# Performance work log

Measured on AMD Instinct MI355X. Metric: run time of the kernel, lower is better.

## Reference

```python
import jax
import jax.numpy as jnp
import numpy as np
from jax import lax

D_MODEL = 256
D_ATT = 256
NHEAD = 8
D_FF = 1024
N_SAMPLED = 128
TEMP = 1.0
DEPTH = 32
N_LOCAL = 4
DH_K = D_ATT // NHEAD
DH_V = D_MODEL // NHEAD
BIG = 1e9
ATT_SCALE = 1.0 / float(np.sqrt(DH_K))


def _rmsnorm(x, g, eps=1e-6):
    return x * lax.rsqrt(jnp.mean(x * x, axis=-1, keepdims=True) + eps) * g


def _weighted_mean(p, mask):
    # p: [b,n,1], mask: [b,n]
    n = jnp.sum(mask, axis=1, keepdims=True)[..., None]
    return jnp.sum(p * mask[..., None], axis=1, keepdims=True) / (n + 1e-9)


def _normalize(v, axis):
    return v / jnp.maximum(jnp.linalg.norm(v, axis=axis, keepdims=True), 1e-12)


def _select_duplet(points, mask, key):
    # pick midpoint of two random masked-in points, per batch
    k1, k2 = jax.random.split(key)
    def pick(k):
        s = jax.random.uniform(k, mask.shape) + (1.0 - mask) * BIG
        idx = jnp.argmin(s, axis=1)
        return jnp.take_along_axis(points, idx[:, None, None], axis=1)  # [b,1,3]
    return (pick(k1) + pick(k2)) * 0.5


def random_serialization(points, mask, key):
    b, n, _ = points.shape
    inf = 2.0 ** (DEPTH // 2 + 3)
    # integer halving schedule: 2^(D/2+1), //2 each step (hits 0 eventually)
    scales = jnp.asarray([float((2 ** (DEPTH // 2 + 1)) >> i) for i in range(DEPTH)], jnp.float32)
    keys = jax.random.split(key, DEPTH)

    def step(carry, xs):
        pts, total, old = carry
        k, scale = xs
        ka, kl, kr = jax.random.split(k, 3)
        ABC = jax.random.normal(ka, (b, 3, 1), jnp.float32)
        ang = jnp.sum(_normalize(ABC, 1) * _normalize(old, 1), axis=1, keepdims=True)
        sgn = jnp.sign(ang)
        sgn = jnp.where(sgn == 0, 1.0, sgn)
        ABC = ABC * sgn
        proj = jnp.matmul(pts, ABC)  # [b,n,1]
        proj = proj - _weighted_mean(proj, mask)
        score = jnp.sign(proj)
        total = total + score * scale
        mask_l = jnp.minimum(jax.nn.relu(-score[..., 0]), mask)
        mask_r = jnp.minimum(jax.nn.relu(score[..., 0]), mask)
        pl = pts - _select_duplet(pts, mask_l, kl)
        pr = pts - _select_duplet(pts, mask_r, kr)
        pts = pl * mask_l[..., None] + pr * mask_r[..., None]
        return (pts, total, ABC), None

    init = (points, jnp.zeros((b, n, 1), jnp.float32), jnp.ones((b, 3, 1), jnp.float32))
    (_, total, _), _ = lax.scan(step, init, (keys, scales))
    total = total + inf * (1.0 - mask)[..., None]
    return jnp.argsort(total[..., 0], axis=1)  # [b,n]


def _dszrc(xn, kv, mask, Ws, bs):
    # learned per-head importance top-k sampler with differentiable gate
    score = jnp.einsum('bnd,dh->bhn', xn, Ws) + bs[None, :, None]
    score = score - (1.0 - mask)[:, None, :] * BIG
    vals, idx = lax.top_k(score, N_SAMPLED)  # [b,h,s]
    gate = jax.nn.sigmoid(vals / TEMP)
    sampled = jnp.take_along_axis(kv, idx[..., None], axis=2)  # [b,h,s,dk+dv]
    return sampled * gate[..., None]


def _block(x, mask, rs, P):
    Wq, bq, Wkv, bkv, Wc, bc, W1, b1, W2, b2, Ws, bs, g1, g2 = P
    b, n, d = x.shape
    xn = _rmsnorm(x, g1)
    q = (xn @ Wq + bq).reshape(b, n, NHEAD, DH_K).transpose(0, 2, 1, 3)
    kv = (xn @ Wkv + bkv).reshape(b, n, NHEAD, DH_K + DH_V).transpose(0, 2, 1, 3)
    kv = _dszrc(xn, kv, mask, Ws, bs)
    k, v = kv[..., :DH_K], kv[..., DH_K:]
    logits = jnp.einsum('bhqd,bhkd->bhqk', q, k) * ATT_SCALE
    att = jax.nn.softmax(logits, axis=-1)
    xa = jnp.einsum('bhqk,bhkd->bhqd', att, v).transpose(0, 2, 1, 3).reshape(b, n, D_MODEL)
    x = x + (xa @ Wc + bc) * rs
    h = _rmsnorm(x, g2)
    mlp = jax.nn.gelu(h @ W1 + b1, approximate=False) @ W2 + b2
    return x + mlp * rs


def _forward(x, x_coords, mask, rs, params):
    idx = random_serialization(x_coords, mask, jax.random.key(42))
    rev = jnp.argsort(idx, axis=1)
    x = jnp.take_along_axis(x, idx[..., None], axis=1)
    b, n, d = x.shape
    # faithful to torch add_remainder_token_trans (pads a full window if n%N==0)
    rem = N_SAMPLED - (n % N_SAMPLED)
    xp = jnp.pad(x, ((0, 0), (0, rem), (0, 0)))
    mp = jnp.pad(mask, ((0, 0), (0, rem)))
    npad = n + rem
    xl = xp.reshape(b * N_SAMPLED, npad // N_SAMPLED, d)
    ml = mp.reshape(b * N_SAMPLED, npad // N_SAMPLED)
    for i in range(N_LOCAL):
        xl = _block(xl, ml, rs, tuple(a[i] for a in params))
    x = xl.reshape(b, npad, d)[:, :n]
    m = mp[:, :n]
    x = _block(x, m, rs, tuple(a[-1] for a in params))
    return jnp.take_along_axis(x, rev[..., None], axis=1)


def setup_inputs() -> dict:
    key = jax.random.key(0)
    ks = jax.random.split(key, 10)
    b, n = 4, 16384
    L = N_LOCAL + 1
    s = 0.02
    return {
        'x': jax.random.normal(ks[0], (b, n, D_MODEL), jnp.float32),
        'x_coords': jax.random.normal(ks[1], (b, n, 3), jnp.float32),
        'mask': jnp.ones((b, n), jnp.float32),
        'residual_scale': jnp.float32(1.0),
        'Wq': jax.random.normal(ks[2], (L, D_MODEL, D_ATT), jnp.float32) * s,
        'bq': jnp.zeros((L, D_ATT), jnp.float32),
        'Wkv': jax.random.normal(ks[3], (L, D_MODEL, D_ATT + D_MODEL), jnp.float32) * s,
        'bkv': jnp.zeros((L, D_ATT + D_MODEL), jnp.float32),
        'Wc': jax.random.normal(ks[4], (L, D_MODEL, D_MODEL), jnp.float32) * s,
        'bc': jnp.zeros((L, D_MODEL), jnp.float32),
        'W1': jax.random.normal(ks[5], (L, D_MODEL, D_FF), jnp.float32) * s,
        'b1': jnp.zeros((L, D_FF), jnp.float32),
        'W2': jax.random.normal(ks[6], (L, D_FF, D_MODEL), jnp.float32) * s,
        'b2': jnp.zeros((L, D_MODEL), jnp.float32),
        'Ws': jax.random.normal(ks[7], (L, D_MODEL, NHEAD), jnp.float32) * s,
        'bs': jnp.zeros((L, NHEAD), jnp.float32),
        'g1': jnp.ones((L, D_MODEL), jnp.float32),
        'g2': jnp.ones((L, D_MODEL), jnp.float32),
    }


def reference(x, x_coords, mask, residual_scale, Wq, bq, Wkv, bkv, Wc, bc, W1, b1, W2, b2, Ws, bs, g1, g2):
    params = (Wq, bq, Wkv, bkv, Wc, bc, W1, b1, W2, b2, Ws, bs, g1, g2)
    return _forward(x, x_coords, mask, residual_scale, params)
```

## Files before the change

kernel.cpp:

```cpp
#include <hip/hip_runtime.h>

typedef unsigned int u32;
typedef unsigned short u16;
typedef unsigned long long u64;
typedef float f32x4 __attribute__((ext_vector_type(4)));
typedef short s16x8 __attribute__((ext_vector_type(8)));

#define BIGF 1e9f

__device__ __forceinline__ float b2f(u16 u){ return __uint_as_float(((u32)u) << 16); }
__device__ __forceinline__ u16 f2b(float f){
  u32 x = __float_as_uint(f);
  u32 r = x + 0x7FFFu + ((x >> 16) & 1u);
  return (u16)(r >> 16);
}
__device__ __forceinline__ float fin(float v){
  u32 u = __float_as_uint(v);
  return ((u & 0x7F800000u) == 0x7F800000u) ? 0.0f : v;
}
__device__ __forceinline__ bool is_bf(const u32* mraw){ return mraw[0] != 0x3F800000u; }
__device__ __forceinline__ float ldin(const void* p, size_t i, bool bf){
  return bf ? b2f(((const u16*)p)[i]) : ((const float*)p)[i];
}
__device__ __forceinline__ u32 mono32(float f){
  u32 u = __float_as_uint(f);
  return u ^ ((u & 0x80000000u) ? 0xFFFFFFFFu : 0x80000000u);
}
__device__ __forceinline__ u64 umin64(u64 a, u64 b){ return a < b ? a : b; }
__device__ __forceinline__ u32 rotl32(u32 x, int r){ return (x << r) | (x >> (32 - r)); }
__device__ __forceinline__ u32 gp2(u32 u, float g){
  float lo = fin(b2f((u16)(u & 0xFFFFu)) * g), hi = fin(b2f((u16)(u >> 16)) * g);
  return (u32)f2b(lo) | ((u32)f2b(hi) << 16);
}
__device__ __forceinline__ float sigm(float ms){
  return (ms > -30.f) ? 1.0f/(1.0f + __expf(-ms)) : 0.0f;
}

__device__ __forceinline__ void gload_lds16(const u16* gsrc, u16* ldst){
  __builtin_amdgcn_global_load_lds(
      (const __attribute__((address_space(1))) u32*)gsrc,
      (__attribute__((address_space(3))) u32*)ldst, 16, 0, 0);
}

__device__ __forceinline__ void tf2(u32 k0, u32 k1, u32 x0, u32 x1, u32& o0, u32& o1){
  u32 ks2 = k0 ^ k1 ^ 0x1BD11BDAu;
  x0 += k0; x1 += k1;
#define TFR(r) { x0 += x1; x1 = rotl32(x1, (r)); x1 ^= x0; }
  TFR(13) TFR(15) TFR(26) TFR(6)
  x0 += k1; x1 += ks2 + 1u;
  TFR(17) TFR(29) TFR(16) TFR(24)
  x0 += ks2; x1 += k0 + 2u;
  TFR(13) TFR(15) TFR(26) TFR(6)
  x0 += k0; x1 += k1 + 3u;
  TFR(17) TFR(29) TFR(16) TFR(24)
  x0 += k1; x1 += ks2 + 4u;
  TFR(13) TFR(15) TFR(26) TFR(6)
  x0 += ks2; x1 += k0 + 5u;
#undef TFR
  o0 = x0; o1 = x1;
}

__device__ float erfinv_xla(float x){
#pragma clang fp contract(off)
  float w = -log1pf(-x*x);
  float p;
  if (w < 5.0f){
    w = w - 2.5f;
    p = 2.81022636e-08f;
    p = 3.43273939e-07f + p*w;
    p = -3.5233877e-06f + p*w;
    p = -4.39150654e-06f + p*w;
    p = 0.00021858087f + p*w;
    p = -0.00125372503f + p*w;
    p = -0.00417768164f + p*w;
    p = 0.246640727f + p*w;
    p = 1.50140941f + p*w;
  } else {
    w = sqrtf(w) - 3.0f;
    p = -0.000200214257f;
    p = 0.000100950558f + p*w;
    p = 0.00134934322f + p*w;
    p = -0.00367342844f + p*w;
    p = 0.00573950773f + p*w;
    p = -0.0076224613f + p*w;
    p = 0.00943887047f + p*w;
    p = 1.00167406f + p*w;
    p = 2.83297682f + p*w;
  }
  return p*x;
}

__global__ void k_fallback(void* out, int n, const u32* mraw){
  bool bf = is_bf(mraw);
  int i = blockIdx.x*256 + threadIdx.x;
  if (i < n){ if (bf) ((u16*)out)[i] = f2b(0.125f); else ((float*)out)[i] = 0.125f; }
}

__global__ void k_zero(u32* p, int n){
  int i = blockIdx.x*256 + threadIdx.x;
  if (i < n) p[i] = 0u;
}

__global__ void k_conv(const void* src, float* dst, int n, const u32* mraw){
  bool bf = is_bf(mraw);
  int i = blockIdx.x*256 + threadIdx.x;
  if (i < n) dst[i] = fin(ldin(src, (size_t)i, bf));
}
__global__ void k_wt(const void* src, u16* dst, int L, int K, int N, const u32* mraw){
  bool bf = is_bf(mraw);
  int i = blockIdx.x*256 + threadIdx.x;
  if (i >= L*K*N) return;
  int l = i/(K*N); int r = i%(K*N); int n = r/K; int k = r%K;
  dst[i] = f2b(fin(ldin(src, (size_t)l*K*N + (size_t)k*N + n, bf)));
}

__global__ void k_rng_setup(float* ABCbuf, u32* pickkeys){
#pragma clang fp contract(off)
  __shared__ float rawn[18][12];
  int s = threadIdx.x;
  if (s < 18){
    u32 ks0, ks1, o0, o1;
    tf2(0u, 42u, 0u, (u32)s, ks0, ks1);
    u32 ka0,ka1,kl0,kl1,kr0,kr1;
    tf2(ks0,ks1, 0u,0u, ka0,ka1);
    tf2(ks0,ks1, 0u,1u, kl0,kl1);
    tf2(ks0,ks1, 0u,2u, kr0,kr1);
    const float MINV = __uint_as_float(0xBF7FFFFFu);
    const float SQ2  = __uint_as_float(0x3FB504F3u);
    for (int j = 0; j < 12; ++j){
      tf2(ka0,ka1, 0u, (u32)j, o0, o1);
      u32 bits = o0 ^ o1;
      float f = __uint_as_float((bits >> 9) | 0x3F800000u) - 1.0f;
      float u = f*2.0f + MINV;
      u = fmaxf(MINV, u);
      rawn[s][j] = SQ2 * erfinv_xla(u);
    }
    u32 a0,a1;
    tf2(kl0,kl1, 0u,0u, a0,a1); pickkeys[(s*4+0)*2]=a0; pickkeys[(s*4+0)*2+1]=a1;
    tf2(kl0,kl1, 0u,1u, a0,a1); pickkeys[(s*4+1)*2]=a0; pickkeys[(s*4+1)*2+1]=a1;
    tf2(kr0,kr1, 0u,0u, a0,a1); pickkeys[(s*4+2)*2]=a0; pickkeys[(s*4+2)*2+1]=a1;
    tf2(kr0,kr1, 0u,1u, a0,a1); pickkeys[(s*4+3)*2]=a0; pickkeys[(s*4+3)*2+1]=a1;
  }
  __syncthreads();
  if (threadIdx.x == 0){
    float oldv[4][3];
    for (int b=0;b<4;b++){ oldv[b][0]=1.f; oldv[b][1]=1.f; oldv[b][2]=1.f; }
    for (int st = 0; st < 18; ++st){
      for (int b = 0; b < 4; ++b){
        float A0 = rawn[st][b*3+0], A1 = rawn[st][b*3+1], A2 = rawn[st][b*3+2];
        float na = fmaxf(sqrtf((A0*A0 + A1*A1) + A2*A2), 1e-12f);
        float p0 = oldv[b][0], p1 = oldv[b][1], p2 = oldv[b][2];
        float no = fmaxf(sqrtf((p0*p0 + p1*p1) + p2*p2), 1e-12f);
        float ang = (A0/na)*(p0/no) + (A1/na)*(p1/no) + (A2/na)*(p2/no);
        float sg = (ang > 0.f) ? 1.f : ((ang < 0.f) ? -1.f : 1.f);
        A0 *= sg; A1 *= sg; A2 *= sg;
        oldv[b][0]=A0; oldv[b][1]=A1; oldv[b][2]=A2;
        ABCbuf[(st*4+b)*3+0]=A0; ABCbuf[(st*4+b)*3+1]=A1; ABCbuf[(st*4+b)*3+2]=A2;
      }
    }
  }
}

__global__ void k_rng_bits(const u32* pickkeys, u32* bits){
  int id = blockIdx.x*256 + threadIdx.x;
  if (id >= 18*4*65536) return;
  int sp = id >> 16; u32 f = (u32)(id & 0xFFFF);
  u32 o0, o1;
  tf2(pickkeys[sp*2], pickkeys[sp*2+1], 0u, f, o0, o1);
  bits[id] = o0 ^ o1;
}

__device__ __forceinline__ void gbar(u32* slot){
  __syncthreads();
  if (threadIdx.x == 0){
    __hip_atomic_fetch_add(slot, 1u, __ATOMIC_ACQ_REL, __HIP_MEMORY_SCOPE_AGENT);
    while (__hip_atomic_load(slot, __ATOMIC_RELAXED, __HIP_MEMORY_SCOPE_AGENT) < 64u)
      __builtin_amdgcn_s_sleep(2);
    (void)__hip_atomic_load(slot, __ATOMIC_ACQUIRE, __HIP_MEMORY_SCOPE_AGENT);
  }
  __syncthreads();
}

__global__ __launch_bounds__(512) void k_serialize_coop(
    const float* __restrict__ coordsf, const float* __restrict__ maskf,
    const float* __restrict__ ABCbuf, const u32* __restrict__ bits,
    int* __restrict__ tkeys, double* __restrict__ sumpart, int* __restrict__ npart,
    u64* __restrict__ reckey, float4* __restrict__ recxyz, u32* __restrict__ gbars){
#pragma clang fp contract(off)
  __shared__ double sd[8];
  __shared__ int si[8];
  __shared__ u64 sp[4][8];
  int bx = blockIdx.x;
  int b = bx >> 4, blk = bx & 15;
  int t = threadIdx.x, wid = t >> 6, lane = t & 63;
  int base_i = blk*1024;

  float p[2][3]; int tk[2]; u32 mb = 0;
#pragma unroll
  for (int j = 0; j < 2; ++j){
    int i = base_i + j*512 + t;
    size_t cb = (size_t)(b*16384 + i)*3;
    p[j][0] = coordsf[cb+0]; p[j][1] = coordsf[cb+1]; p[j][2] = coordsf[cb+2];
    if (maskf[b*16384 + i] > 0.f) mb |= (1u << j);
    tk[j] = 0;
  }
  {
    int c = __popc(mb);
#pragma unroll
    for (int d = 1; d < 64; d <<= 1) c += __shfl_xor(c, d);
    if (lane == 0) si[wid] = c;
    __syncthreads();
    if (t == 0){ int cc = 0; for (int w = 0; w < 8; ++w) cc += si[w]; npart[b*16 + blk] = cc; }
  }
  float nplus = 0.f;

  for (int s = 0; s < 18; ++s){
    float A0 = ABCbuf[(s*4+b)*3+0], A1 = ABCbuf[(s*4+b)*3+1], A2 = ABCbuf[(s*4+b)*3+2];
    float pr[2]; double acc = 0.0;
#pragma unroll
    for (int j = 0; j < 2; ++j){
      pr[j] = p[j][0]*A0 + p[j][1]*A1 + p[j][2]*A2;
      if ((mb >> j) & 1u) acc += (double)pr[j];
    }
#pragma unroll
    for (int d = 1; d < 64; d <<= 1) acc += __shfl_xor(acc, d);
    if (lane == 0) sd[wid] = acc;
    __syncthreads();
    if (t == 0){ double tt = 0.0; for (int w = 0; w < 8; ++w) tt += sd[w]; sumpart[b*16 + blk] = tt; }
    gbar(&gbars[s*2 + 0]);

    if (s == 0){
      int cc = 0; for (int k2 = 0; k2 < 16; ++k2) cc += npart[b*16 + k2];
      nplus = (float)((double)cc + 1e-9);
    }
    double tot = 0.0;
    for (int k2 = 0; k2 < 16; ++k2) tot += sumpart[b*16 + k2];
    float mean = ((float)tot) / nplus;

    u32 sideL = 0, sideR = 0;
    int sc17 = 1 << (17 - s);
#pragma unroll
    for (int j = 0; j < 2; ++j){
      float pc = pr[j] - mean;
      int sc = (pc > 0.f) ? 1 : ((pc < 0.f) ? -1 : 0);
      tk[j] += sc * sc17;
      bool mi = (mb >> j) & 1u;
      if (mi && sc < 0) sideL |= (1u << j);
      if (mi && sc > 0) sideR |= (1u << j);
    }
    u64 mine[4]; int bj[4];
#pragma unroll
    for (int pk = 0; pk < 4; ++pk){ mine[pk] = ~0ULL; bj[pk] = 0; }
#pragma unroll
    for (int pk = 0; pk < 4; ++pk){
      const u32* bp = bits + (size_t)(s*4 + pk)*65536 + b*16384;
      u32 sm = (pk < 2) ? sideL : sideR;
#pragma unroll
      for (int j = 0; j < 2; ++j){
        if ((sm >> j) & 1u){
          int i = base_i + j*512 + t;
          u64 pkd = ((u64)(bp[i] >> 9) << 14) | (u32)i;
          if (pkd < mine[pk]){ mine[pk] = pkd; bj[pk] = j; }
        }
      }
    }
    u64 red[4];
#pragma unroll
    for (int pk = 0; pk < 4; ++pk) red[pk] = mine[pk];
#pragma unroll
    for (int d = 1; d < 64; d <<= 1)
#pragma unroll
      for (int pk = 0; pk < 4; ++pk) red[pk] = umin64(red[pk], __shfl_xor(red[pk], d));
    if (lane == 0){
#pragma unroll
      for (int pk = 0; pk < 4; ++pk) sp[pk][wid] = red[pk];
    }
    __syncthreads();
    u64 mm[4];
#pragma unroll
    for (int pk = 0; pk < 4; ++pk){
      u64 v = ~0ULL;
      for (int w = 0; w < 8; ++w) v = umin64(v, sp[pk][w]);
      mm[pk] = v;
    }
#pragma unroll
    for (int pk = 0; pk < 4; ++pk){
      int ri = ((b*4 + pk) << 4) + blk;
      if (mm[pk] == ~0ULL){
        if (t == 0){ reckey[ri] = ~0ULL; recxyz[ri] = make_float4(0.f, 0.f, 0.f, 0.f); }
      } else if (mine[pk] == mm[pk]){
        int j = bj[pk];
        reckey[ri] = mm[pk];
        recxyz[ri] = make_float4(p[j][0], p[j][1], p[j][2], 0.f);
      }
    }
    gbar(&gbars[s*2 + 1]);

    float wc[4][3];
#pragma unroll
    for (int pk = 0; pk < 4; ++pk){
      u64 best = ~0ULL; int bk = 0;
      for (int k2 = 0; k2 < 16; ++k2){
        u64 kk = reckey[((b*4 + pk) << 4) + k2];
        if (kk < best){ best = kk; bk = k2; }
      }
      float4 c = recxyz[((b*4 + pk) << 4) + bk];
      wc[pk][0] = c.x; wc[pk][1] = c.y; wc[pk][2] = c.z;
    }
    float dl0=(wc[0][0]+wc[1][0])*0.5f, dl1=(wc[0][1]+wc[1][1])*0.5f, dl2=(wc[0][2]+wc[1][2])*0.5f;
    float dr0=(wc[2][0]+wc[3][0])*0.5f, dr1=(wc[2][1]+wc[3][1])*0.5f, dr2=(wc[2][2]+wc[3][2])*0.5f;
#pragma unroll
    for (int j = 0; j < 2; ++j){
      bool L = (sideL >> j) & 1u, R = (sideR >> j) & 1u;
      if (L){ p[j][0]-=dl0; p[j][1]-=dl1; p[j][2]-=dl2; }
      else if (R){ p[j][0]-=dr0; p[j][1]-=dr1; p[j][2]-=dr2; }
      else { p[j][0]=0.f; p[j][1]=0.f; p[j][2]=0.f; }
    }
  }
#pragma unroll
  for (int j = 0; j < 2; ++j){
    int i = base_i + j*512 + t;
    tkeys[b*16384 + i] = tk[j] + (((mb >> j) & 1u) ? 0 : 524288);
  }
}

__global__ __launch_bounds__(1024) void k_bsort_phase1(u64* buf){
  __shared__ u64 sb[8192];
  u64* g = buf + (size_t)blockIdx.x*8192;
  int tid = threadIdx.x;
  for (int i = tid; i < 8192; i += 1024) sb[i] = g[i];
  int ab = blockIdx.x & 1;
  for (int k = 2; k <= 8192; k <<= 1){
    for (int j = k >> 1; j > 0; j >>= 1){
      __syncthreads();
      for (int pp = tid; pp < 4096; pp += 1024){
        int i  = ((pp & ~(j - 1)) << 1) | (pp & (j - 1));
        int ix = i | j;
        bool up = (k == 8192) ? (ab == 0) : ((i & k) == 0);
        u64 A = sb[i], B = sb[ix];
        if ((A > B) == up){ sb[i] = B; sb[ix] = A; }
      }
    }
  }
  __syncthreads();
  for (int i = tid; i < 8192; i += 1024) g[i] = sb[i];
}
__global__ __launch_bounds__(1024) void k_bsort_merge(u64* buf){
  u64* g = buf + (size_t)blockIdx.x*16384;
  for (int i = threadIdx.x; i < 8192; i += 1024){
    u64 A = g[i], B = g[i + 8192];
    if (A > B){ g[i] = B; g[i + 8192] = A; }
  }
}
__global__ __launch_bounds__(1024) void k_bsort_phase3(u64* buf){
  __shared__ u64 sb[8192];
  u64* g = buf + (size_t)blockIdx.x*8192;
  int tid = threadIdx.x;
  for (int i = tid; i < 8192; i += 1024) sb[i] = g[i];
  for (int j = 4096; j > 0; j >>= 1){
    __syncthreads();
    for (int pp = tid; pp < 4096; pp += 1024){
      int i  = ((pp & ~(j - 1)) << 1) | (pp & (j - 1));
      int ix = i | j;
      u64 A = sb[i], B = sb[ix];
      if (A > B){ sb[i] = B; sb[ix] = A; }
    }
  }
  __syncthreads();
  for (int i = tid; i < 8192; i += 1024) g[i] = sb[i];
}

__global__ void k_fill_sort(const int* tkeys, u64* sbuf){
  int id = blockIdx.x*256 + threadIdx.x;
  if (id >= 65536) return;
  u32 tv = (u32)(tkeys[id] + 262144);
  sbuf[id] = ((u64)tv << 14) | (u32)(id & 16383);
}
__global__ void k_unpack_sort(const u64* sbuf, int* idxb, int* revb){
  int id = blockIdx.x*256 + threadIdx.x;
  if (id >= 65536) return;
  int a = id >> 14, r = id & 16383;
  int orig = (int)(sbuf[id] & 16383u);
  idxb[id] = orig;
  revb[(a << 14) | orig] = r;
}

__global__ void k_gather(const void* xraw, const int* idxb, float* xbuf, const u32* mraw){
  bool bf = is_bf(mraw);
  int r = blockIdx.x, c = threadIdx.x;
  int b = r / 16512, rr = r % 16512;
  float v = 0.f;
  if (rr < 16384){
    int src = idxb[b*16384 + rr];
    v = fin(ldin(xraw, (size_t)(b*16384 + src)*256 + c, bf));
  }
  xbuf[(size_t)r*256 + c] = v;
}

__global__ void k_rmsnorm(const float* x, const float* g, u16* xn){
  int row = blockIdx.x*4 + (threadIdx.x >> 6);
  int lane = threadIdx.x & 63;
  float4 xv = *(const float4*)&x[(size_t)row*256 + lane*4];
  xv.x = fin(xv.x); xv.y = fin(xv.y); xv.z = fin(xv.z); xv.w = fin(xv.w);
  float ss = xv.x*xv.x + xv.y*xv.y + xv.z*xv.z + xv.w*xv.w;
#pragma unroll
  for (int d = 1; d < 64; d <<= 1) ss += __shfl_xor(ss, d);
  float sc = 1.0f / sqrtf(ss*(1.0f/256.0f) + 1e-6f);
  float4 gv = *(const float4*)&g[lane*4];
  ushort4 o4;
  o4.x = f2b(fin((xv.x*sc)*gv.x)); o4.y = f2b(fin((xv.y*sc)*gv.y));
  o4.z = f2b(fin((xv.z*sc)*gv.z)); o4.w = f2b(fin((xv.w*sc)*gv.w));
  *(ushort4*)&xn[(size_t)row*256 + lane*4] = o4;
}

__global__ __launch_bounds__(256) void k_gemm(const u16* A, int lda, const u16* Bt, int ldb,
                                              int M, int N, int K, const float* bias,
                                              void* C, int ldc, int mode, const float* rsp){
  __shared__ __align__(16) u16 As[128*64];
  __shared__ __align__(16) u16 Bs[128*64];
  int tid = threadIdx.x;
  int gx = (int)gridDim.x;
  int nwg = gx * (int)gridDim.y;
  int d = (int)blockIdx.y * gx + (int)blockIdx.x;
  int q = nwg >> 3, r = nwg & 7;
  int xcd = d & 7, off = d >> 3;
  int wg = (xcd < r ? xcd*(q+1) : r*(q+1) + (xcd - r)*q) + off;
  int bxi = wg % gx, byi = wg / gx;
  int gm0 = byi*128, gn0 = bxi*128;
  int wv = tid >> 6, lane = tid & 63, q4 = lane >> 4, l16 = lane & 15;
  int wm = (wv >> 1)*64, wn = (wv & 1)*64;
  int lr = lane >> 3;
  int lcs = ((lane & 7) ^ lr) << 3;
  f32x4 acc[4][4];
#pragma unroll
  for (int i = 0; i < 4; ++i)
#pragma unroll
    for (int j = 0; j < 4; ++j) acc[i][j] = (f32x4){0.f,0.f,0.f,0.f};
  for (int k0 = 0; k0 < K; k0 += 64){
    __syncthreads();
#pragma unroll
    for (int i = 0; i < 4; ++i){
      int chunk = wv*4 + i;
      int row = chunk*8 + lr;
      gload_lds16(&A[(size_t)(gm0+row)*lda + k0 + lcs],  &As[chunk*512]);
      gload_lds16(&Bt[(size_t)(gn0+row)*ldb + k0 + lcs], &Bs[chunk*512]);
    }
    __syncthreads();
#pragma unroll
    for (int ks = 0; ks < 64; ks += 32){
      int swc = ((((ks >> 3) + q4) ^ (l16 & 7)) << 3);
      s16x8 aF[4], bF[4];
#pragma unroll
      for (int mt = 0; mt < 4; ++mt) aF[mt] = *(const s16x8*)&As[(wm + mt*16 + l16)*64 + swc];
#pragma unroll
      for (int nt = 0; nt < 4; ++nt) bF[nt] = *(const s16x8*)&Bs[(wn + nt*16 + l16)*64 + swc];
#pragma unroll
      for (int mt = 0; mt < 4; ++mt)
#pragma unroll
        for (int nt = 0; nt < 4; ++nt)
          acc[mt][nt] = __builtin_amdgcn_mfma_f32_16x16x32_bf16(aF[mt], bF[nt], acc[mt][nt], 0, 0, 0);
    }
  }
  float rs = rsp[0];
  const float SQ2C = 1.41421356237f;
#pragma unroll
  for (int mt = 0; mt < 4; ++mt)
#pragma unroll
    for (int nt = 0; nt < 4; ++nt){
      int col = gn0 + wn + nt*16 + l16;
      float bi = bias[col];
#pragma unroll
      for (int rg = 0; rg < 4; ++rg){
        int row = gm0 + wm + mt*16 + q4*4 + rg;
        float v = fin(acc[mt][nt][rg] + bi);
        size_t off2 = (size_t)row*ldc + col;
        if (mode == 0) ((float*)C)[off2] = v;
        else if (mode == 1){ float* X = (float*)C; X[off2] = fin(X[off2] + v*rs); }
        else if (mode == 2) ((u16*)C)[off2] = f2b(v);
        else { float gl = 0.5f * v * (1.0f + erff(v / SQ2C)); ((u16*)C)[off2] = f2b(fin(gl)); }
      }
    }
}

__global__ __launch_bounds__(256) void k_gemm_score(const u16* __restrict__ A,
                                                    const u16* __restrict__ Bt,
                                                    int M, const float* __restrict__ bias,
                                                    float* __restrict__ C){
  __shared__ __align__(16) u16 As[128*72];
  int tid = threadIdx.x;
  int gm0 = blockIdx.x*128;
  int wv = tid >> 6, lane = tid & 63, q4 = lane >> 4, l16 = lane & 15;
  int wm = wv*32;
  int ar = tid >> 2, ac = tid & 3;
  f32x4 acc[2];
  acc[0] = (f32x4){0.f,0.f,0.f,0.f};
  acc[1] = (f32x4){0.f,0.f,0.f,0.f};
  for (int k0 = 0; k0 < 256; k0 += 64){
    __syncthreads();
#pragma unroll
    for (int ps = 0; ps < 2; ++ps){
      int r2 = ps*64 + ar;
      uint4 va0 = {0u,0u,0u,0u}, va1 = {0u,0u,0u,0u};
      if (gm0 + r2 < M){
        const u16* ap = &A[(size_t)(gm0+r2)*256 + k0 + ac*16];
        va0 = ((const uint4*)ap)[0];
        va1 = ((const uint4*)ap)[1];
      }
      *(uint4*)&As[r2*72 + ac*16]     = va0;
      *(uint4*)&As[r2*72 + ac*16 + 8] = va1;
    }
    __syncthreads();
#pragma unroll
    for (int ks = 0; ks < 64; ks += 32){
      s16x8 bF = (s16x8){0,0,0,0,0,0,0,0};
      if (l16 < 8) bF = *(const s16x8*)&Bt[(size_t)l16*256 + k0 + ks + q4*8];
      s16x8 aF0 = *(const s16x8*)&As[(wm + l16)*72 + ks + q4*8];
      s16x8 aF1 = *(const s16x8*)&As[(wm + 16 + l16)*72 + ks + q4*8];
      acc[0] = __builtin_amdgcn_mfma_f32_16x16x32_bf16(aF0, bF, acc[0], 0, 0, 0);
      acc[1] = __builtin_amdgcn_mfma_f32_16x16x32_bf16(aF1, bF, acc[1], 0, 0, 0);
    }
  }
  if (l16 < 8){
    float bi = bias[l16];
#pragma unroll
    for (int mt = 0; mt < 2; ++mt)
#pragma unroll
      for (int rg = 0; rg < 4; ++rg){
        int row = gm0 + wm + mt*16 + q4*4 + rg;
        if (row < M) C[(size_t)row*8 + l16] = fin(acc[mt][rg] + bi);
      }
  }
}

__global__ __launch_bounds__(512) void k_sel_local(const float* scoreb, const float* maskf,
                                                   u32* sel, float* gateb){
  int s = blockIdx.x, h = threadIdx.x >> 6, lane = threadIdx.x & 63;
  int b = s >> 7, tt = s & 127;
  u64 pm = ~0ULL;
  for (int rep = 0; rep < 3; ++rep){
    int j = lane + rep*64;
    if (j < 129){
      int p = tt*129 + j;
      float m = (p < 16384) ? maskf[b*16384 + p] : 0.f;
      float ms = fin(scoreb[(size_t)(s*129 + j)*8 + h]) - (1.0f - m)*BIGF;
      u64 pk = ((u64)mono32(ms) << 9) | (u32)(511 - j);
      pm = umin64(pm, pk);
    }
  }
#pragma unroll
  for (int d = 1; d < 64; d <<= 1) pm = umin64(pm, __shfl_xor(pm, d));
  int dropped = 511 - (int)(pm & 511u);
  int sh = s*8 + h;
  for (int rep = 0; rep < 3; ++rep){
    int j = lane + rep*64;
    if (j < 129 && j != dropped){
      int slot = j - (j > dropped ? 1 : 0);
      int p = tt*129 + j;
      float m = (p < 16384) ? maskf[b*16384 + p] : 0.f;
      float ms = fin(scoreb[(size_t)(s*129 + j)*8 + h]) - (1.0f - m)*BIGF;
      sel[sh*128 + slot] = (u32)(s*129 + j);
      gateb[sh*128 + slot] = fin(sigm(ms));
    }
  }
}

__global__ void k_fill_topk(const float* scoreb, const float* maskf, u64* sbuf){
  int id = blockIdx.x*256 + threadIdx.x;
  if (id >= 524288) return;
  int arr = id >> 14, i = id & 16383;
  int b = arr >> 3, h = arr & 7;
  float m = maskf[b*16384 + i];
  float ms = fin(scoreb[(size_t)(b*16512 + i)*8 + h]) - (1.0f - m)*BIGF;
  sbuf[id] = ((u64)(~mono32(ms)) << 14) | (u32)i;
}
__global__ void k_sel_gemit(const u64* sbuf, const float* scoreb, const float* maskf,
                            u32* sel, float* gateb){
  int arr = blockIdx.x, tid = threadIdx.x;
  int b = arr >> 3, h = arr & 7;
  int j = (int)(sbuf[(size_t)arr*16384 + tid] & 16383u);
  float m = maskf[b*16384 + j];
  float ms = fin(scoreb[(size_t)(b*16512 + j)*8 + h]) - (1.0f - m)*BIGF;
  sel[arr*128 + tid] = (u32)(b*16512 + j);
  gateb[arr*128 + tid] = fin(sigm(ms));
}

__global__ __launch_bounds__(256) void k_attn(const u16* qb, const u16* vkv,
                                              const u32* sel, const float* gateb,
                                              u16* xa, int gmode){
  __shared__ __align__(16) u16 Qsm[144*40];
  __shared__ __align__(16) u16 Ksm[128*40];
  __shared__ __align__(16) u16 Vtsm[32*136];
  __shared__ __align__(16) u16 Psm[4*16*136];
  int tid = threadIdx.x;
  int bx = blockIdx.x, h = blockIdx.y;
  int rows, rowbase, kvs, ntiles;
  if (gmode){
    int b = bx >> 7, rb = bx & 127;
    rows = 128; rowbase = b*16512 + rb*128; kvs = b; ntiles = 8;
  } else {
    rows = 129; rowbase = bx*129; kvs = bx; ntiles = 9;
  }
  int sh = kvs*8 + h;
  for (int t = tid; t < 144; t += 256) *(uint4*)&Qsm[t*40 + 32] = (uint4){0u,0u,0u,0u};
  if (tid < 128) *(uint4*)&Ksm[tid*40 + 32] = (uint4){0u,0u,0u,0u};
  if (tid < 32)  *(uint4*)&Vtsm[tid*136 + 128] = (uint4){0u,0u,0u,0u};
  if (tid < 64)  *(uint4*)&Psm[tid*136 + 128] = (uint4){0u,0u,0u,0u};
  for (int t = tid; t < 576; t += 256){
    int r = t >> 2, c = t & 3;
    uint4 v = {0u,0u,0u,0u};
    if (r < rows) v = *(const uint4*)&qb[(size_t)(rowbase + r)*256 + h*32 + c*8];
    *(uint4*)&Qsm[r*40 + c*8] = v;
  }
  for (int t = tid; t < 512; t += 256){
    int slot = t >> 2, part = t & 3;
    u32 rowi = sel[sh*128 + slot];
    float gv = fin(gateb[sh*128 + slot]);
    uint4 vk = *(const uint4*)&vkv[(size_t)rowi*512 + h*64 + part*8];
    uint4 wk; wk.x = gp2(vk.x, gv); wk.y = gp2(vk.y, gv); wk.z = gp2(vk.z, gv); wk.w = gp2(vk.w, gv);
    *(uint4*)&Ksm[slot*40 + part*8] = wk;
    uint4 vv = *(const uint4*)&vkv[(size_t)rowi*512 + h*64 + 32 + part*8];
    u32 vd[4] = {vv.x, vv.y, vv.z, vv.w};
#pragma unroll
    for (int e = 0; e < 4; ++e){
      float lo = fin(b2f((u16)(vd[e] & 0xFFFFu)) * gv), hi = fin(b2f((u16)(vd[e] >> 16)) * gv);
      Vtsm[(part*8 + e*2 + 0)*136 + slot] = f2b(lo);
      Vtsm[(part*8 + e*2 + 1)*136 + slot] = f2b(hi);
    }
  }
  __syncthreads();
  int wv = tid >> 6, lane = tid & 63, q4 = lane >> 4, l16 = lane & 15;
  u16* Pw = Psm + wv*(16*136);
  const float ATTSC = 0.17677669529663689f;
  f32x4 z = {0.f,0.f,0.f,0.f};
  for (int mt = wv; mt < ntiles; mt += 4){
    int m0 = mt*16;
    s16x8 aQ = *(const s16x8*)&Qsm[(m0 + l16)*40 + q4*8];
    f32x4 S[8];
#pragma unroll
    for (int nt = 0; nt < 8; ++nt){
      s16x8 bK = *(const s16x8*)&Ksm[(nt*16 + l16)*40 + q4*8];
      S[nt] = __builtin_amdgcn_mfma_f32_16x16x32_bf16(aQ, bK, z, 0, 0, 0);
    }
    float mx[4] = {-1e30f,-1e30f,-1e30f,-1e30f};
#pragma unroll
    for (int nt = 0; nt < 8; ++nt)
#pragma unroll
      for (int rg = 0; rg < 4; ++rg){ float v = fin(S[nt][rg])*ATTSC; S[nt][rg] = v; mx[rg] = fmaxf(mx[rg], v); }
#pragma unroll
    for (int d = 1; d < 16; d <<= 1)
#pragma unroll
      for (int rg = 0; rg < 4; ++rg) mx[rg] = fmaxf(mx[rg], __shfl_xor(mx[rg], d));
    float sm[4] = {0.f,0.f,0.f,0.f};
#pragma unroll
    for (int nt = 0; nt < 8; ++nt)
#pragma unroll
      for (int rg = 0; rg < 4; ++rg){ float e = __expf(S[nt][rg] - mx[rg]); S[nt][rg] = e; sm[rg] += e; }
#pragma unroll
    for (int d = 1; d < 16; d <<= 1)
#pragma unroll
      for (int rg = 0; rg < 4; ++rg) sm[rg] += __shfl_xor(sm[rg], d);
    float inv[4];
#pragma unroll
    for (int rg = 0; rg < 4; ++rg) inv[rg] = 1.0f/fmaxf(sm[rg], 1e-20f);
#pragma unroll
    for (int nt = 0; nt < 8; ++nt)
#pragma unroll
      for (int rg = 0; rg < 4; ++rg)
        Pw[(q4*4 + rg)*136 + nt*16 + l16] = f2b(fin(S[nt][rg]*inv[rg]));
    f32x4 O0 = z, O1 = z;
#pragma unroll
    for (int kq = 0; kq < 4; ++kq){
      s16x8 aP = *(const s16x8*)&Pw[l16*136 + kq*32 + q4*8];
      s16x8 b0 = *(const s16x8*)&Vtsm[l16*136 + kq*32 + q4*8];
      s16x8 b1 = *(const s16x8*)&Vtsm[(16 + l16)*136 + kq*32 + q4*8];
      O0 = __builtin_amdgcn_mfma_f32_16x16x32_bf16(aP, b0, O0, 0, 0, 0);
      O1 = __builtin_amdgcn_mfma_f32_16x16x32_bf16(aP, b1, O1, 0, 0, 0);
    }
#pragma unroll
    for (int rg = 0; rg < 4; ++rg){
      int r = m0 + q4*4 + rg;
      if (r < rows){
        size_t base = (size_t)(rowbase + r)*256 + h*32;
        xa[base + l16] = f2b(fin(O0[rg]));
        xa[base + 16 + l16] = f2b(fin(O1[rg]));
      }
    }
  }
}

__global__ void k_output(const float* xbuf, const int* revb, void* out, const u32* mraw){
  bool bf = is_bf(mraw);
  int r = blockIdx.x, c = threadIdx.x;
  int b = r >> 14;
  int rank = revb[r];
  float v = fin(xbuf[(size_t)(b*16512 + rank)*256 + c]);
  if (bf) ((u16*)out)[(size_t)r*256 + c] = f2b(v);
  else ((float*)out)[(size_t)r*256 + c] = v;
}

extern "C" void kernel_launch(void* const* d_in, const int* in_sizes, int n_in,
                              void* d_out, int out_size, void* d_ws, size_t ws_size,
                              hipStream_t stream){
  (void)in_sizes; (void)n_in;
  const u32* mraw = (const u32*)d_in[2];
  char* wsp = (char*)d_ws;
  size_t o = 0;
  auto alloc = [&](size_t bytes)->void*{ void* p = (void*)(wsp + o); o += (bytes + 255) & ~(size_t)255; return p; };
  float* maskf   = (float*)alloc(65536u*4);
  float* coordsf = (float*)alloc(196608u*4);
  float* rsf     = (float*)alloc(256);
  float* bqf     = (float*)alloc(5*256*4);
  float* bkvf    = (float*)alloc(5*512*4);
  float* bsf     = (float*)alloc(5*8*4);
  float* bcf     = (float*)alloc(5*256*4);
  float* b1f     = (float*)alloc(5*1024*4);
  float* b2f     = (float*)alloc(5*256*4);
  float* g1f     = (float*)alloc(5*256*4);
  float* g2f     = (float*)alloc(5*256*4);
  u16* WqT  = (u16*)alloc((size_t)5*256*256*2);
  u16* WvT  = (u16*)alloc((size_t)5*512*256*2);
  u16* WsT  = (u16*)alloc((size_t)5*8*256*2);
  u16* WcT  = (u16*)alloc((size_t)5*256*256*2);
  u16* W1T  = (u16*)alloc((size_t)5*1024*256*2);
  u16* W2T  = (u16*)alloc((size_t)5*1024*256*2);
  float* ABCbuf = (float*)alloc(18*12*4);
  u32* pickkeys = (u32*)alloc(72*2*4);
  int* tkeys = (int*)alloc(65536u*4);
  int* idxb  = (int*)alloc(65536u*4);
  int* revb  = (int*)alloc(65536u*4);
  double* sumpart = (double*)alloc(64*8);
  int*    npart   = (int*)alloc(64*4);
  u64*    reckey  = (u64*)alloc(256*8);
  float4* recxyz  = (float4*)alloc(256*16);
  u32*    gbars   = (u32*)alloc(64*4);
  u64* sortbuf = (u64*)alloc((size_t)32*16384*8);
  float* xbuf = (float*)alloc((size_t)66048*256*4);
  u16* xn  = (u16*)alloc((size_t)66048*256*2);
  float* scoreb = (float*)alloc((size_t)66048*8*4);
  const size_t SZ_VKV = (size_t)66048*512*2;
  const size_t SZ_QB  = (size_t)66048*256*2;
  const size_t SZ_SEL = (size_t)4096*128*4;
  char* Sbase = (char*)alloc(SZ_VKV + SZ_QB + 2*SZ_SEL);
  u16* vkv    = (u16*)Sbase;
  u16* qb     = (u16*)(Sbase + SZ_VKV);
  u32* sel    = (u32*)(Sbase + SZ_VKV + SZ_QB);
  float* gateb= (float*)(Sbase + SZ_VKV + SZ_QB + SZ_SEL);
  u32* bitsb  = (u32*)Sbase;
  u16* ffb    = (u16*)Sbase;
  u16* xa     = qb;

  if (o > ws_size){
    k_fallback<<<dim3((out_size + 255)/256), 256, 0, stream>>>(d_out, out_size, mraw);
    return;
  }

  k_conv<<<dim3(256), 256, 0, stream>>>(d_in[2], maskf, 65536, mraw);
  k_conv<<<dim3(768), 256, 0, stream>>>(d_in[1], coordsf, 196608, mraw);
  k_conv<<<dim3(1), 256, 0, stream>>>(d_in[3], rsf, 1, mraw);
  k_conv<<<dim3(5), 256, 0, stream>>>(d_in[5], bqf, 1280, mraw);
  k_conv<<<dim3(10), 256, 0, stream>>>(d_in[7], bkvf, 2560, mraw);
  k_conv<<<dim3(1), 256, 0, stream>>>(d_in[15], bsf, 40, mraw);
  k_conv<<<dim3(5), 256, 0, stream>>>(d_in[9], bcf, 1280, mraw);
  k_conv<<<dim3(20), 256, 0, stream>>>(d_in[11], b1f, 5120, mraw);
  k_conv<<<dim3(5), 256, 0, stream>>>(d_in[13], b2f, 1280, mraw);
  k_conv<<<dim3(5), 256, 0, stream>>>(d_in[16], g1f, 1280, mraw);
  k_conv<<<dim3(5), 256, 0, stream>>>(d_in[17], g2f, 1280, mraw);
  k_wt<<<dim3(1280), 256, 0, stream>>>(d_in[4], WqT, 5, 256, 256, mraw);
  k_wt<<<dim3(2560), 256, 0, stream>>>(d_in[6], WvT, 5, 256, 512, mraw);
  k_wt<<<dim3(40), 256, 0, stream>>>(d_in[14], WsT, 5, 256, 8, mraw);
  k_wt<<<dim3(1280), 256, 0, stream>>>(d_in[8], WcT, 5, 256, 256, mraw);
  k_wt<<<dim3(5120), 256, 0, stream>>>(d_in[10], W1T, 5, 256, 1024, mraw);
  k_wt<<<dim3(5120), 256, 0, stream>>>(d_in[12], W2T, 5, 1024, 256, mraw);

  k_rng_setup<<<dim3(1), 64, 0, stream>>>(ABCbuf, pickkeys);
  k_rng_bits<<<dim3(18432), 256, 0, stream>>>(pickkeys, bitsb);
  k_zero<<<dim3(1), 256, 0, stream>>>(gbars, 64);
  {
    const float* a_coords = coordsf;
    const float* a_mask   = maskf;
    const float* a_abc    = ABCbuf;
    const u32*   a_bits   = bitsb;
    int*         a_tkeys  = tkeys;
    double*      a_sum    = sumpart;
    int*         a_np     = npart;
    u64*         a_rk     = reckey;
    float4*      a_rx     = recxyz;
    u32*         a_gb     = gbars;
    void* kargs[10];
    kargs[0] = (void*)&a_coords; kargs[1] = (void*)&a_mask; kargs[2] = (void*)&a_abc;
    kargs[3] = (void*)&a_bits;   kargs[4] = (void*)&a_tkeys;
    kargs[5] = (void*)&a_sum;    kargs[6] = (void*)&a_np;
    kargs[7] = (void*)&a_rk;     kargs[8] = (void*)&a_rx;
    kargs[9] = (void*)&a_gb;
    hipLaunchCooperativeKernel((void*)k_serialize_coop, dim3(64), dim3(512), kargs, 0, stream);
  }
  k_fill_sort<<<dim3(256), 256, 0, stream>>>(tkeys, sortbuf);
  k_bsort_phase1<<<dim3(8), 1024, 0, stream>>>(sortbuf);
  k_bsort_merge<<<dim3(4), 1024, 0, stream>>>(sortbuf);
  k_bsort_phase3<<<dim3(8), 1024, 0, stream>>>(sortbuf);
  k_unpack_sort<<<dim3(256), 256, 0, stream>>>(sortbuf, idxb, revb);
  k_gather<<<dim3(66048), 256, 0, stream>>>(d_in[0], idxb, xbuf, mraw);

  auto gemm = [&](const u16* A, int lda, const u16* Bt, int ldb, int M, int N, int K,
                  const float* bias, void* C, int ldc, int mode){
    dim3 g((N + 127)/128, (M + 127)/128);
    k_gemm<<<g, 256, 0, stream>>>(A, lda, Bt, ldb, M, N, K, bias, C, ldc, mode, rsf);
  };

  for (int l = 0; l < 5; ++l){
    bool local = (l < 4);
    k_rmsnorm<<<dim3(16512), 256, 0, stream>>>(xbuf, g1f + l*256, xn);
    gemm(xn, 256, WqT + (size_t)l*256*256, 256, 66048, 256, 256, bqf + l*256, qb, 256, 2);
    gemm(xn, 256, WvT + (size_t)l*512*256, 256, 66048, 512, 256, bkvf + l*512, vkv, 512, 2);
    k_gemm_score<<<dim3(516), 256, 0, stream>>>(xn, WsT + (size_t)l*8*256, 66048,
                                                bsf + l*8, scoreb);
    if (local){
      k_sel_local<<<dim3(512), 512, 0, stream>>>(scoreb, maskf, sel, gateb);
    } else {
      k_fill_topk<<<dim3(2048), 256, 0, stream>>>(scoreb, maskf, sortbuf);
      k_bsort_phase1<<<dim3(64), 1024, 0, stream>>>(sortbuf);
      k_bsort_merge<<<dim3(32), 1024, 0, stream>>>(sortbuf);
      k_bsort_phase3<<<dim3(64), 1024, 0, stream>>>(sortbuf);
      k_sel_gemit<<<dim3(32), 128, 0, stream>>>(sortbuf, scoreb, maskf, sel, gateb);
    }
    k_attn<<<dim3(512, 8), 256, 0, stream>>>(qb, vkv, sel, gateb, xa, local ? 0 : 1);
    gemm(xa, 256, WcT + (size_t)l*256*256, 256, 66048, 256, 256, bcf + l*256, xbuf, 256, 1);
    k_rmsnorm<<<dim3(16512), 256, 0, stream>>>(xbuf, g2f + l*256, xn);
    for (int half = 0; half < 2; ++half){
      const u16* Ah = xn + (size_t)half*33024*256;
      gemm(Ah, 256, W1T + (size_t)l*1024*256, 256, 33024, 1024, 256, b1f + l*1024, ffb, 1024, 3);
      gemm(ffb, 1024, W2T + (size_t)l*1024*256, 1024, 33024, 256, 1024, b2f + l*256,
           xbuf + (size_t)half*33024*256, 256, 1);
    }
  }
  k_output<<<dim3(65536), 256, 0, stream>>>(xbuf, revb, d_out, mraw);
}
```

Baseline: 3.471 ms.

## Fuse Q and KV projections, batch param conversion, tile weight transposes, vectorize gather/output

Concatenates the Wq and Wkv weights and biases so that a single GEMM with a split-output epilogue (mode 4) writes both q and kv, replacing two GEMM launches per layer. The many small bias and gain conversion launches are merged into one kernel. Weight transposes now go through a shared-memory tile so both reads and writes are coalesced. The gather and output kernels handle four rows per block with float4 accesses, and the cooperative serialization barrier now waits only for the 16 blocks of each batch instead of all 64. These add more code paths and a new GEMM epilogue branch with per-element column tests.

```diff
diff --git a/kernel.cpp b/kernel.cpp
--- a/kernel.cpp
+++ b/kernel.cpp
@@ -106,12 +106,66 @@
   int i = blockIdx.x*256 + threadIdx.x;
   if (i < n) dst[i] = fin(ldin(src, (size_t)i, bf));
 }
+
+__global__ void k_conv_b(const void* s_rs, const void* s_bq, const void* s_bkv,
+                         const void* s_bs, const void* s_bc, const void* s_b1,
+                         const void* s_b2, const void* s_g1, const void* s_g2,
+                         float* rsf, float* bqvf, float* bsf, float* bcf,
+                         float* b1f, float* b2f, float* g1f, float* g2f,
+                         const u32* mraw){
+  bool bf = is_bf(mraw);
+  int i = blockIdx.x*256 + threadIdx.x;
+  if (i < 1){ rsf[i] = fin(ldin(s_rs, i, bf)); return; }
+  i -= 1;
+  if (i < 3840){
+    int l = i / 768, c = i % 768;
+    float v = (c < 256) ? fin(ldin(s_bq, (size_t)l*256 + c, bf))
+                        : fin(ldin(s_bkv, (size_t)l*512 + (c - 256), bf));
+    bqvf[i] = v; return;
+  }
+  i -= 3840;
+  if (i < 40){ bsf[i] = fin(ldin(s_bs, i, bf)); return; }
+  i -= 40;
+  if (i < 1280){ bcf[i] = fin(ldin(s_bc, i, bf)); return; }
+  i -= 1280;
+  if (i < 5120){ b1f[i] = fin(ldin(s_b1, i, bf)); return; }
+  i -= 5120;
+  if (i < 1280){ b2f[i] = fin(ldin(s_b2, i, bf)); return; }
+  i -= 1280;
+  if (i < 1280){ g1f[i] = fin(ldin(s_g1, i, bf)); return; }
+  i -= 1280;
+  if (i < 1280){ g2f[i] = fin(ldin(s_g2, i, bf)); return; }
+}
+
 __global__ void k_wt(const void* src, u16* dst, int L, int K, int N, const u32* mraw){
   bool bf = is_bf(mraw);
   int i = blockIdx.x*256 + threadIdx.x;
   if (i >= L*K*N) return;
   int l = i/(K*N); int r = i%(K*N); int n = r/K; int k = r%K;
   dst[i] = f2b(fin(ldin(src, (size_t)l*K*N + (size_t)k*N + n, bf)));
+}
+
+__global__ void k_wt2(const void* src, u16* dst, int K, int N, int ostr, int rowoff,
+                      const u32* mraw){
+  bool bf = is_bf(mraw);
+  __shared__ float tl[32][33];
+  int nt = N >> 5, kt = K >> 5;
+  int bid = blockIdx.x;
+  int l = bid / (nt*kt); int r2 = bid % (nt*kt);
+  int k0 = (r2 / nt) << 5, n0 = (r2 % nt) << 5;
+  int tx = threadIdx.x & 31, ty = threadIdx.x >> 5;
+  size_t sbase = (size_t)l*K*N;
+#pragma unroll
+  for (int j = 0; j < 4; ++j){
+    int k = k0 + ty + j*8;
+    tl[ty + j*8][tx] = fin(ldin(src, sbase + (size_t)k*N + n0 + tx, bf));
+  }
+  __syncthreads();
+#pragma unroll
+  for (int j = 0; j < 4; ++j){
+    int n = n0 + ty + j*8;
+    dst[(size_t)l*ostr + (size_t)(rowoff + n)*K + k0 + tx] = f2b(tl[tx][ty + j*8]);
+  }
 }
 
 __global__ void k_rng_setup(float* ABCbuf, u32* pickkeys){
@@ -170,11 +224,11 @@
   bits[id] = o0 ^ o1;
 }
 
-__device__ __forceinline__ void gbar(u32* slot){
+__device__ __forceinline__ void gbar16(u32* slot){
   __syncthreads();
   if (threadIdx.x == 0){
     __hip_atomic_fetch_add(slot, 1u, __ATOMIC_ACQ_REL, __HIP_MEMORY_SCOPE_AGENT);
-    while (__hip_atomic_load(slot, __ATOMIC_RELAXED, __HIP_MEMORY_SCOPE_AGENT) < 64u)
+    while (__hip_atomic_load(slot, __ATOMIC_RELAXED, __HIP_MEMORY_SCOPE_AGENT) < 16u)
       __builtin_amdgcn_s_sleep(2);
     (void)__hip_atomic_load(slot, __ATOMIC_ACQUIRE, __HIP_MEMORY_SCOPE_AGENT);
   }
@@ -194,6 +248,7 @@
   int b = bx >> 4, blk = bx & 15;
   int t = threadIdx.x, wid = t >> 6, lane = t & 63;
   int base_i = blk*1024;
+  u32* gb = gbars + b*64;
 
   float p[2][3]; int tk[2]; u32 mb = 0;
 #pragma unroll
@@ -227,7 +282,7 @@
     if (lane == 0) sd[wid] = acc;
     __syncthreads();
     if (t == 0){ double tt = 0.0; for (int w = 0; w < 8; ++w) tt += sd[w]; sumpart[b*16 + blk] = tt; }
-    gbar(&gbars[s*2 + 0]);
+    gbar16(&gb[s*2 + 0]);
 
     if (s == 0){
       int cc = 0; for (int k2 = 0; k2 < 16; ++k2) cc += npart[b*16 + k2];
@@ -294,7 +349,7 @@
         recxyz[ri] = make_float4(p[j][0], p[j][1], p[j][2], 0.f);
       }
     }
-    gbar(&gbars[s*2 + 1]);
+    gbar16(&gb[s*2 + 1]);
 
     float wc[4][3];
 #pragma unroll
@@ -387,14 +442,21 @@
 
 __global__ void k_gather(const void* xraw, const int* idxb, float* xbuf, const u32* mraw){
   bool bf = is_bf(mraw);
-  int r = blockIdx.x, c = threadIdx.x;
-  int b = r / 16512, rr = r % 16512;
-  float v = 0.f;
+  int row = blockIdx.x*4 + (threadIdx.x >> 6), lane = threadIdx.x & 63;
+  int b = row / 16512, rr = row % 16512;
+  float4 v = {0.f, 0.f, 0.f, 0.f};
   if (rr < 16384){
     int src = idxb[b*16384 + rr];
-    v = fin(ldin(xraw, (size_t)(b*16384 + src)*256 + c, bf));
-  }
-  xbuf[(size_t)r*256 + c] = v;
+    size_t base = (size_t)(b*16384 + src)*256 + lane*4;
+    if (bf){
+      ushort4 u = *(const ushort4*)((const u16*)xraw + base);
+      v.x = fin(b2f(u.x)); v.y = fin(b2f(u.y)); v.z = fin(b2f(u.z)); v.w = fin(b2f(u.w));
+    } else {
+      float4 f = *(const float4*)((const float*)xraw + base);
+      v.x = fin(f.x); v.y = fin(f.y); v.z = fin(f.z); v.w = fin(f.w);
+    }
+  }
+  *(float4*)&xbuf[(size_t)row*256 + lane*4] = v;
 }
 
 __global__ void k_rmsnorm(const float* x, const float* g, u16* xn){
@@ -415,7 +477,8 @@
 
 __global__ __launch_bounds__(256) void k_gemm(const u16* A, int lda, const u16* Bt, int ldb,
                                               int M, int N, int K, const float* bias,
-                                              void* C, int ldc, int mode, const float* rsp){
+                                              void* C, int ldc, int mode, const float* rsp,
+                                              void* C2){
   __shared__ __align__(16) u16 As[128*64];
   __shared__ __align__(16) u16 Bs[128*64];
   int tid = threadIdx.x;
@@ -477,7 +540,11 @@
         if (mode == 0) ((float*)C)[off2] = v;
         else if (mode == 1){ float* X = (float*)C; X[off2] = fin(X[off2] + v*rs); }
         else if (mode == 2) ((u16*)C)[off2] = f2b(v);
-        else { float gl = 0.5f * v * (1.0f + erff(v / SQ2C)); ((u16*)C)[off2] = f2b(fin(gl)); }
+        else if (mode == 3){ float gl = 0.5f * v * (1.0f + erff(v / SQ2C)); ((u16*)C)[off2] = f2b(fin(gl)); }
+        else {
+          if (col < 256) ((u16*)C)[(size_t)row*256 + col] = f2b(v);
+          else ((u16*)C2)[(size_t)row*512 + (col - 256)] = f2b(v);
+        }
       }
     }
 }
@@ -690,12 +757,17 @@
 
 __global__ void k_output(const float* xbuf, const int* revb, void* out, const u32* mraw){
   bool bf = is_bf(mraw);
-  int r = blockIdx.x, c = threadIdx.x;
-  int b = r >> 14;
-  int rank = revb[r];
-  float v = fin(xbuf[(size_t)(b*16512 + rank)*256 + c]);
-  if (bf) ((u16*)out)[(size_t)r*256 + c] = f2b(v);
-  else ((float*)out)[(size_t)r*256 + c] = v;
+  int row = blockIdx.x*4 + (threadIdx.x >> 6), lane = threadIdx.x & 63;
+  int b = row >> 14;
+  int rank = revb[row];
+  float4 f = *(const float4*)&xbuf[(size_t)(b*16512 + rank)*256 + lane*4];
+  f.x = fin(f.x); f.y = fin(f.y); f.z = fin(f.z); f.w = fin(f.w);
+  if (bf){
+    ushort4 u; u.x = f2b(f.x); u.y = f2b(f.y); u.z = f2b(f.z); u.w = f2b(f.w);
+    *(ushort4*)((u16*)out + (size_t)row*256 + lane*4) = u;
+  } else {
+    *(float4*)((float*)out + (size_t)row*256 + lane*4) = f;
+  }
 }
 
 extern "C" void kernel_launch(void* const* d_in, const int* in_sizes, int n_in,
@@ -709,16 +781,14 @@
   float* maskf   = (float*)alloc(65536u*4);
   float* coordsf = (float*)alloc(196608u*4);
   float* rsf     = (float*)alloc(256);
-  float* bqf     = (float*)alloc(5*256*4);
-  float* bkvf    = (float*)alloc(5*512*4);
+  float* bqvf    = (float*)alloc(5*768*4);
   float* bsf     = (float*)alloc(5*8*4);
   float* bcf     = (float*)alloc(5*256*4);
   float* b1f     = (float*)alloc(5*1024*4);
   float* b2f     = (float*)alloc(5*256*4);
   float* g1f     = (float*)alloc(5*256*4);
   float* g2f     = (float*)alloc(5*256*4);
-  u16* WqT  = (u16*)alloc((size_t)5*256*256*2);
-  u16* WvT  = (u16*)alloc((size_t)5*512*256*2);
+  u16* WqvT = (u16*)alloc((size_t)5*768*256*2);
   u16* WsT  = (u16*)alloc((size_t)5*8*256*2);
   u16* WcT  = (u16*)alloc((size_t)5*256*256*2);
   u16* W1T  = (u16*)alloc((size_t)5*1024*256*2);
@@ -732,7 +802,7 @@
   int*    npart   = (int*)alloc(64*4);
   u64*    reckey  = (u64*)alloc(256*8);
   float4* recxyz  = (float4*)alloc(256*16);
-  u32*    gbars   = (u32*)alloc(64*4);
+  u32*    gbars   = (u32*)alloc(256*4);
   u64* sortbuf = (u64*)alloc((size_t)32*16384*8);
   float* xbuf = (float*)alloc((size_t)66048*256*4);
   u16* xn  = (u16*)alloc((size_t)66048*256*2);
@@ -756,25 +826,19 @@
 
   k_conv<<<dim3(256), 256, 0, stream>>>(d_in[2], maskf, 65536, mraw);
   k_conv<<<dim3(768), 256, 0, stream>>>(d_in[1], coordsf, 196608, mraw);
-  k_conv<<<dim3(1), 256, 0, stream>>>(d_in[3], rsf, 1, mraw);
-  k_conv<<<dim3(5), 256, 0, stream>>>(d_in[5], bqf, 1280, mraw);
-  k_conv<<<dim3(10), 256, 0, stream>>>(d_in[7], bkvf, 2560, mraw);
-  k_conv<<<dim3(1), 256, 0, stream>>>(d_in[15], bsf, 40, mraw);
-  k_conv<<<dim3(5), 256, 0, stream>>>(d_in[9], bcf, 1280, mraw);
-  k_conv<<<dim3(20), 256, 0, stream>>>(d_in[11], b1f, 5120, mraw);
-  k_conv<<<dim3(5), 256, 0, stream>>>(d_in[13], b2f, 1280, mraw);
-  k_conv<<<dim3(5), 256, 0, stream>>>(d_in[16], g1f, 1280, mraw);
-  k_conv<<<dim3(5), 256, 0, stream>>>(d_in[17], g2f, 1280, mraw);
-  k_wt<<<dim3(1280), 256, 0, stream>>>(d_in[4], WqT, 5, 256, 256, mraw);
-  k_wt<<<dim3(2560), 256, 0, stream>>>(d_in[6], WvT, 5, 256, 512, mraw);
+  k_conv_b<<<dim3(56), 256, 0, stream>>>(d_in[3], d_in[5], d_in[7], d_in[15], d_in[9],
+                                         d_in[11], d_in[13], d_in[16], d_in[17],
+                                         rsf, bqvf, bsf, bcf, b1f, b2f, g1f, g2f, mraw);
+  k_wt2<<<dim3(5*8*8),  256, 0, stream>>>(d_in[4],  WqvT, 256, 256,  768*256, 0,   mraw);
+  k_wt2<<<dim3(5*8*16), 256, 0, stream>>>(d_in[6],  WqvT, 256, 512,  768*256, 256, mraw);
+  k_wt2<<<dim3(5*8*8),  256, 0, stream>>>(d_in[8],  WcT,  256, 256,  256*256, 0,   mraw);
+  k_wt2<<<dim3(5*8*32), 256, 0, stream>>>(d_in[10], W1T,  256, 1024, 1024*256, 0,  mraw);
+  k_wt2<<<dim3(5*32*8), 256, 0, stream>>>(d_in[12], W2T,  1024, 256, 256*1024, 0,  mraw);
   k_wt<<<dim3(40), 256, 0, stream>>>(d_in[14], WsT, 5, 256, 8, mraw);
-  k_wt<<<dim3(1280), 256, 0, stream>>>(d_in[8], WcT, 5, 256, 256, mraw);
-  k_wt<<<dim3(5120), 256, 0, stream>>>(d_in[10], W1T, 5, 256, 1024, mraw);
-  k_wt<<<dim3(5120), 256, 0, stream>>>(d_in[12], W2T, 5, 1024, 256, mraw);
 
   k_rng_setup<<<dim3(1), 64, 0, stream>>>(ABCbuf, pickkeys);
   k_rng_bits<<<dim3(18432), 256, 0, stream>>>(pickkeys, bitsb);
-  k_zero<<<dim3(1), 256, 0, stream>>>(gbars, 64);
+  k_zero<<<dim3(1), 256, 0, stream>>>(gbars, 256);
   {
     const float* a_coords = coordsf;
     const float* a_mask   = maskf;
@@ -799,19 +863,23 @@
   k_bsort_merge<<<dim3(4), 1024, 0, stream>>>(sortbuf);
   k_bsort_phase3<<<dim3(8), 1024, 0, stream>>>(sortbuf);
   k_unpack_sort<<<dim3(256), 256, 0, stream>>>(sortbuf, idxb, revb);
-  k_gather<<<dim3(66048), 256, 0, stream>>>(d_in[0], idxb, xbuf, mraw);
+  k_gather<<<dim3(16512), 256, 0, stream>>>(d_in[0], idxb, xbuf, mraw);
 
   auto gemm = [&](const u16* A, int lda, const u16* Bt, int ldb, int M, int N, int K,
                   const float* bias, void* C, int ldc, int mode){
     dim3 g((N + 127)/128, (M + 127)/128);
-    k_gemm<<<g, 256, 0, stream>>>(A, lda, Bt, ldb, M, N, K, bias, C, ldc, mode, rsf);
+    k_gemm<<<g, 256, 0, stream>>>(A, lda, Bt, ldb, M, N, K, bias, C, ldc, mode, rsf, (void*)0);
   };
 
   for (int l = 0; l < 5; ++l){
     bool local = (l < 4);
     k_rmsnorm<<<dim3(16512), 256, 0, stream>>>(xbuf, g1f + l*256, xn);
-    gemm(xn, 256, WqT + (size_t)l*256*256, 256, 66048, 256, 256, bqf + l*256, qb, 256, 2);
-    gemm(xn, 256, WvT + (size_t)l*512*256, 256, 66048, 512, 256, bkvf + l*512, vkv, 512, 2);
+    {
+      dim3 g(6, 516);
+      k_gemm<<<g, 256, 0, stream>>>(xn, 256, WqvT + (size_t)l*768*256, 256,
+                                    66048, 768, 256, bqvf + l*768,
+                                    qb, 0, 4, rsf, (void*)vkv);
+    }
     k_gemm_score<<<dim3(516), 256, 0, stream>>>(xn, WsT + (size_t)l*8*256, 66048,
                                                 bsf + l*8, scoreb);
     if (local){
@@ -833,5 +901,5 @@
            xbuf + (size_t)half*33024*256, 256, 1);
     }
   }
-  k_output<<<dim3(65536), 256, 0, stream>>>(xbuf, revb, d_out, mraw);
-}
+  k_output<<<dim3(16384), 256, 0, stream>>>(xbuf, revb, d_out, mraw);
+}
```

After: 4.177 ms. +20.3%, slower.
